# Performance work log

Measured on AMD Instinct MI355X. Metric: run time of the kernel, lower is better.

Reference implementation:

```python
import jax, jax.numpy as jnp
import numpy as np

N0, N1, N2 = 100000, 300000, 200000
C = 64
SLOPE = 0.2

NNZ_A0, NNZ_A1, NNZ_C2, NNZ_B1, NNZ_B2 = 600000, 1200000, 600000, 600000, 600000


def _seg_softmax(logits, seg, n):
    # softmax over nonzero entries of each row (segment = row index)
    m = jax.ops.segment_max(logits, seg, num_segments=n)
    e = jnp.exp(logits - m[seg])
    s = jax.ops.segment_sum(e, seg, num_segments=n)
    return e / s[seg]


def _hbs(x, rows, cols, W, a, n):
    # Higher-order attention block, same rank (m_hop=1, A values = 1)
    m = x @ W                                   # [n, out]
    out = W.shape[1]
    logits = jax.nn.leaky_relu((m @ a[:out])[rows] + (m @ a[out:])[cols], SLOPE)
    att = _seg_softmax(logits, rows, n)         # row-wise softmax on sparsity pattern
    return jax.ops.segment_sum(att[:, None] * m[cols], rows, num_segments=n)


def _hbns(xs, xt, t_rows, s_cols, Ws, Wt, a, n_s, n_t):
    # Higher-order attention block between ranks; neighborhood is [n_t, n_s]
    sm = xs @ Ws                                # [n_s, t_out]
    tm = xt @ Wt                                # [n_t, s_out]
    t_out, s_out = Ws.shape[1], Wt.shape[1]
    # e: source -> target attention logits (row = target); cat([sm_j, tm_i]) @ a
    e = jax.nn.leaky_relu((sm @ a[:t_out])[s_cols] + (tm @ a[t_out:])[t_rows], SLOPE)
    # f: target -> source attention logits (row = source); cat([tm_i, sm_j]) @ a
    f = jax.nn.leaky_relu((tm @ a[:s_out])[t_rows] + (sm @ a[s_out:])[s_cols], SLOPE)
    att_st = _seg_softmax(e, t_rows, n_t)
    att_ts = _seg_softmax(f, s_cols, n_s)
    msg_t = jax.ops.segment_sum(att_st[:, None] * sm[s_cols], t_rows, num_segments=n_t)
    msg_s = jax.ops.segment_sum(att_ts[:, None] * tm[t_rows], s_cols, num_segments=n_s)
    return msg_s, msg_t


def setup_inputs() -> dict:
    key = jax.random.key(0)
    ks = iter(jax.random.split(key, 64))
    sc = 1.0 / np.sqrt(C)
    d = {
        "x_0": jax.random.normal(next(ks), (N0, C), jnp.float32),
        "x_1": jax.random.normal(next(ks), (N1, C), jnp.float32),
        "x_2": jax.random.normal(next(ks), (N2, C), jnp.float32),
        "adj0_rows": jax.random.randint(next(ks), (NNZ_A0,), 0, N0, jnp.int32),
        "adj0_cols": jax.random.randint(next(ks), (NNZ_A0,), 0, N0, jnp.int32),
        "adj1_rows": jax.random.randint(next(ks), (NNZ_A1,), 0, N1, jnp.int32),
        "adj1_cols": jax.random.randint(next(ks), (NNZ_A1,), 0, N1, jnp.int32),
        "coadj2_rows": jax.random.randint(next(ks), (NNZ_C2,), 0, N2, jnp.int32),
        "coadj2_cols": jax.random.randint(next(ks), (NNZ_C2,), 0, N2, jnp.int32),
        "inc1_rows": jax.random.randint(next(ks), (NNZ_B1,), 0, N0, jnp.int32),
        "inc1_cols": jax.random.randint(next(ks), (NNZ_B1,), 0, N1, jnp.int32),
        "inc2_rows": jax.random.randint(next(ks), (NNZ_B2,), 0, N1, jnp.int32),
        "inc2_cols": jax.random.randint(next(ks), (NNZ_B2,), 0, N2, jnp.int32),
    }
    for nm in ["W_hbs0_l1", "W_hbs0_l2", "W_hbs1_l2", "W_hbs2_l2",
               "Ws01_l1", "Wt01_l1", "Ws12_l1", "Wt12_l1",
               "Ws01_l2", "Wt01_l2", "Ws12_l2", "Wt12_l2"]:
        d[nm] = jax.random.normal(next(ks), (C, C), jnp.float32) * sc
    for nm in ["a_hbs0_l1", "a_hbs0_l2", "a_hbs1_l2", "a_hbs2_l2",
               "a01_l1", "a12_l1", "a01_l2", "a12_l2"]:
        d[nm] = jax.random.normal(next(ks), (2 * C,), jnp.float32) * sc
    return d


def reference(x_0, x_1, x_2,
              adj0_rows, adj0_cols, adj1_rows, adj1_cols,
              coadj2_rows, coadj2_cols, inc1_rows, inc1_cols,
              inc2_rows, inc2_cols,
              W_hbs0_l1, a_hbs0_l1, W_hbs0_l2, a_hbs0_l2,
              W_hbs1_l2, a_hbs1_l2, W_hbs2_l2, a_hbs2_l2,
              Ws01_l1, Wt01_l1, a01_l1, Ws12_l1, Wt12_l1, a12_l1,
              Ws01_l2, Wt01_l2, a01_l2, Ws12_l2, Wt12_l2, a12_l2):
    # ---- level 1 ----
    x_0_to_0 = _hbs(x_0, adj0_rows, adj0_cols, W_hbs0_l1, a_hbs0_l1, N0)
    x_0_to_1, x_1_to_0 = _hbns(x_1, x_0, inc1_rows, inc1_cols,
                               Ws01_l1, Wt01_l1, a01_l1, N1, N0)
    x_1_to_2, x_2_to_1 = _hbns(x_2, x_1, inc2_rows, inc2_cols,
                               Ws12_l1, Wt12_l1, a12_l1, N2, N1)
    x_0_l1 = x_0_to_0 + x_1_to_0
    x_1_l1 = x_0_to_1 + x_2_to_1
    x_2_l1 = x_1_to_2
    # ---- level 2 ----
    x_0_to_0 = _hbs(x_0_l1, adj0_rows, adj0_cols, W_hbs0_l2, a_hbs0_l2, N0)
    x_1_to_1 = _hbs(x_1_l1, adj1_rows, adj1_cols, W_hbs1_l2, a_hbs1_l2, N1)
    x_2_to_2 = _hbs(x_2_l1, coadj2_rows, coadj2_cols, W_hbs2_l2, a_hbs2_l2, N2)
    x_0_to_1, _ = _hbns(x_1_l1, x_0_l1, inc1_rows, inc1_cols,
                        Ws01_l2, Wt01_l2, a01_l2, N1, N0)
    x_1_to_2, _ = _hbns(x_2_l1, x_1_l1, inc2_rows, inc2_cols,
                        Ws12_l2, Wt12_l2, a12_l2, N2, N1)
    x_0_out = x_0_to_0
    x_1_out = x_0_to_1 + x_1_to_1
    x_2_out = x_1_to_2 + x_2_to_2
    return x_0_out, x_1_out, x_2_out
```

## Files before the change

kernel.cpp:

```cpp
#include <hip/hip_runtime.h>

#define CN0 100000
#define CN1 300000
#define CN2 200000
#define EA0 600000
#define EA1 1200000
#define EC2 600000
#define EB1 600000
#define EB2 600000
#define TOTSEG (2*CN0 + 3*CN1 + 2*CN2)
#define OVCAP 16384

typedef __attribute__((ext_vector_type(8))) short short8;
typedef __attribute__((ext_vector_type(4))) float f32x4;
typedef __attribute__((ext_vector_type(4))) unsigned short u16x4;

__device__ __forceinline__ float lrelu(float v) { return v >= 0.f ? v : 0.2f * v; }
__device__ __forceinline__ unsigned short btop(float x) {
    return (unsigned short)(__float_as_uint(x) >> 16);
}
__device__ __forceinline__ unsigned short f2bf(float x) {
    unsigned u = __float_as_uint(x);
    return (unsigned short)((u + 0x7FFFu + ((u >> 16) & 1u)) >> 16);
}
__device__ __forceinline__ float bf2f(unsigned short b) {
    return __uint_as_float((unsigned)b << 16);
}

struct Pats {
    const int* seg[7];
    const int* vidx[7];
    int E[7];
    int base[7];
    int K[7];
    int eoff[7];
};

struct MMJob {
    const float* X; const float* W; const float* a;
    unsigned short* Y; float* p; float* q; int nchunk;
};

__device__ __forceinline__ void mm_body(const float* __restrict__ X, const float* __restrict__ W,
                                        const float* __restrict__ a, unsigned short* __restrict__ Yb,
                                        float* __restrict__ p, float* __restrict__ q,
                                        int nchunk, int wid, int nw, int lane) {
    int l15 = lane & 15, lq = lane >> 4;
    short8 bh[4][2], bl[4][2];
#pragma unroll
    for (int t = 0; t < 4; ++t)
#pragma unroll
        for (int h = 0; h < 2; ++h) {
            const float* wp = W + (size_t)(h * 32 + lq * 8) * 64 + 16 * t + l15;
#pragma unroll
            for (int j = 0; j < 8; ++j) {
                float wv = wp[(size_t)j * 64];
                unsigned short hi = btop(wv);
                float rem = wv - __uint_as_float((unsigned)hi << 16);
                bh[t][h][j] = (short)hi;
                bl[t][h][j] = (short)btop(rem);
            }
        }
    float av0[4], av1[4];
#pragma unroll
    for (int t = 0; t < 4; ++t) {
        av0[t] = a[16 * t + l15];
        av1[t] = a[64 + 16 * t + l15];
    }
    for (int c = wid; c < nchunk; c += nw) {
        int base = c * 16;
        f32x4 acc[4];
#pragma unroll
        for (int t = 0; t < 4; ++t) acc[t] = (f32x4){0.f, 0.f, 0.f, 0.f};
#pragma unroll
        for (int h = 0; h < 2; ++h) {
            const f32x4* xp = (const f32x4*)(X + (size_t)(base + l15) * 64 + h * 32 + lq * 8);
            f32x4 x0 = xp[0], x1 = xp[1];
            short8 ah, al;
#pragma unroll
            for (int j = 0; j < 4; ++j) {
                unsigned short h0 = btop(x0[j]);
                float r0 = x0[j] - __uint_as_float((unsigned)h0 << 16);
                ah[j] = (short)h0;
                al[j] = (short)btop(r0);
                unsigned short h1 = btop(x1[j]);
                float r1 = x1[j] - __uint_as_float((unsigned)h1 << 16);
                ah[4 + j] = (short)h1;
                al[4 + j] = (short)btop(r1);
            }
#pragma unroll
            for (int t = 0; t < 4; ++t) {
                acc[t] = __builtin_amdgcn_mfma_f32_16x16x32_bf16(ah, bh[t][h], acc[t], 0, 0, 0);
                acc[t] = __builtin_amdgcn_mfma_f32_16x16x32_bf16(ah, bl[t][h], acc[t], 0, 0, 0);
                acc[t] = __builtin_amdgcn_mfma_f32_16x16x32_bf16(al, bh[t][h], acc[t], 0, 0, 0);
            }
        }
#pragma unroll
        for (int t = 0; t < 4; ++t)
#pragma unroll
            for (int r = 0; r < 4; ++r)
                Yb[(size_t)(base + lq * 4 + r) * 64 + 16 * t + l15] = f2bf(acc[t][r]);
#pragma unroll
        for (int r = 0; r < 4; ++r) {
            float pr = acc[0][r] * av0[0] + acc[1][r] * av0[1] + acc[2][r] * av0[2] + acc[3][r] * av0[3];
            float qr = acc[0][r] * av1[0] + acc[1][r] * av1[1] + acc[2][r] * av1[2] + acc[3][r] * av1[3];
#pragma unroll
            for (int off = 8; off; off >>= 1) {
                pr += __shfl_xor(pr, off, 64);
                qr += __shfl_xor(qr, off, 64);
            }
            if (l15 == 0) {
                p[base + lq * 4 + r] = pr;
                q[base + lq * 4 + r] = qr;
            }
        }
    }
}

__global__ __launch_bounds__(256) void k_l1_fused(
        MMJob j0, MMJob j1, MMJob j2, MMJob j3, MMJob j4,
        Pats P, int* __restrict__ cnt, int* __restrict__ ell,
        int* __restrict__ ovf_gs, int* __restrict__ ovf_vx, int* __restrict__ ovf_n,
        int mmBlocks) {
    int b = blockIdx.x;
    int nm = 5 * mmBlocks;
    int lane = threadIdx.x & 63;
    if (b < nm) {
        int role = b / mmBlocks, rb = b - role * mmBlocks;
        MMJob J = (role == 0) ? j0 : (role == 1) ? j1 : (role == 2) ? j2
                : (role == 3) ? j3 : j4;
        int wid = rb * (blockDim.x >> 6) + (threadIdx.x >> 6);
        int nw = mmBlocks * (blockDim.x >> 6);
        mm_body(J.X, J.W, J.a, J.Y, J.p, J.q, J.nchunk, wid, nw, lane);
    } else {
        int hb = b - nm;
        int pidx = 0, acc = 0;
        for (; pidx < 7; ++pidx) {
            int pb = (P.E[pidx] + 255) >> 8;
            if (hb < acc + pb) break;
            acc += pb;
        }
        if (pidx >= 7) return;
        int e = (hb - acc) * 256 + threadIdx.x;
        if (e >= P.E[pidx]) return;
        int sv = P.seg[pidx][e];
        int gs = P.base[pidx] + sv;
        int vx = P.vidx[pidx][e];
        int r = atomicAdd(&cnt[gs], 1);
        int Kp = P.K[pidx];
        if (r < Kp) {
            ell[(size_t)P.eoff[pidx] + (size_t)sv * Kp + r] = vx;
        } else {
            int o = atomicAdd(ovf_n, 1);
            if (o < OVCAP) { ovf_gs[o] = gs; ovf_vx[o] = vx; }
        }
    }
}

template <int DUAL, int VEC>
__global__ __launch_bounds__(256) void mm64_t(
        const float* __restrict__ X,
        const float* __restrict__ W1, const float* __restrict__ a1,
        unsigned short* __restrict__ Y1, float* __restrict__ p1, float* __restrict__ q1,
        const float* __restrict__ W2, const float* __restrict__ a2,
        unsigned short* __restrict__ Y2, float* __restrict__ p2, float* __restrict__ q2,
        const float* __restrict__ uuv, float* __restrict__ pv, int nchunk) {
    int lane = threadIdx.x & 63;
    int l15 = lane & 15, lq = lane >> 4;
    int wid = blockIdx.x * (blockDim.x >> 6) + (threadIdx.x >> 6);
    int nw = gridDim.x * (blockDim.x >> 6);

    short8 b1h[4][2], b1l[4][2], b2h[4][2], b2l[4][2];
#pragma unroll
    for (int t = 0; t < 4; ++t)
#pragma unroll
        for (int h = 0; h < 2; ++h) {
            const float* wp = W1 + (size_t)(h * 32 + lq * 8) * 64 + 16 * t + l15;
#pragma unroll
            for (int j = 0; j < 8; ++j) {
                float wv = wp[(size_t)j * 64];
                unsigned short hi = btop(wv);
                float rem = wv - __uint_as_float((unsigned)hi << 16);
                b1h[t][h][j] = (short)hi;
                b1l[t][h][j] = (short)btop(rem);
            }
        }
    if (DUAL) {
#pragma unroll
        for (int t = 0; t < 4; ++t)
#pragma unroll
            for (int h = 0; h < 2; ++h) {
                const float* wp = W2 + (size_t)(h * 32 + lq * 8) * 64 + 16 * t + l15;
#pragma unroll
                for (int j = 0; j < 8; ++j) {
                    float wv = wp[(size_t)j * 64];
                    unsigned short hi = btop(wv);
                    float rem = wv - __uint_as_float((unsigned)hi << 16);
                    b2h[t][h][j] = (short)hi;
                    b2l[t][h][j] = (short)btop(rem);
                }
            }
    }
    float a10[4], a11[4], a20[4], a21[4];
#pragma unroll
    for (int t = 0; t < 4; ++t) {
        a10[t] = a1[16 * t + l15];
        a11[t] = a1[64 + 16 * t + l15];
        if (DUAL) { a20[t] = a2[16 * t + l15]; a21[t] = a2[64 + 16 * t + l15]; }
    }
    float uv[16];
    if (VEC) {
#pragma unroll
        for (int h = 0; h < 2; ++h)
#pragma unroll
            for (int j = 0; j < 8; ++j) uv[h * 8 + j] = uuv[h * 32 + lq * 8 + j];
    }

    for (int c = wid; c < nchunk; c += nw) {
        int base = c * 16;
        f32x4 acc1[4], acc2[4];
#pragma unroll
        for (int t = 0; t < 4; ++t) {
            acc1[t] = (f32x4){0.f, 0.f, 0.f, 0.f};
            if (DUAL) acc2[t] = (f32x4){0.f, 0.f, 0.f, 0.f};
        }
        float vp = 0.f;
#pragma unroll
        for (int h = 0; h < 2; ++h) {
            const f32x4* xp = (const f32x4*)(X + (size_t)(base + l15) * 64 + h * 32 + lq * 8);
            f32x4 x0 = xp[0], x1 = xp[1];
            if (VEC) {
#pragma unroll
                for (int j = 0; j < 4; ++j)
                    vp += x0[j] * uv[h * 8 + j] + x1[j] * uv[h * 8 + 4 + j];
            }
            short8 ah, al;
#pragma unroll
            for (int j = 0; j < 4; ++j) {
                unsigned short h0 = btop(x0[j]);
                float r0 = x0[j] - __uint_as_float((unsigned)h0 << 16);
                ah[j] = (short)h0;
                al[j] = (short)btop(r0);
                unsigned short h1 = btop(x1[j]);
                float r1 = x1[j] - __uint_as_float((unsigned)h1 << 16);
                ah[4 + j] = (short)h1;
                al[4 + j] = (short)btop(r1);
            }
#pragma unroll
            for (int t = 0; t < 4; ++t) {
                acc1[t] = __builtin_amdgcn_mfma_f32_16x16x32_bf16(ah, b1h[t][h], acc1[t], 0, 0, 0);
                acc1[t] = __builtin_amdgcn_mfma_f32_16x16x32_bf16(ah, b1l[t][h], acc1[t], 0, 0, 0);
                acc1[t] = __builtin_amdgcn_mfma_f32_16x16x32_bf16(al, b1h[t][h], acc1[t], 0, 0, 0);
                if (DUAL) {
                    acc2[t] = __builtin_amdgcn_mfma_f32_16x16x32_bf16(ah, b2h[t][h], acc2[t], 0, 0, 0);
                    acc2[t] = __builtin_amdgcn_mfma_f32_16x16x32_bf16(ah, b2l[t][h], acc2[t], 0, 0, 0);
                    acc2[t] = __builtin_amdgcn_mfma_f32_16x16x32_bf16(al, b2h[t][h], acc2[t], 0, 0, 0);
                }
            }
        }
#pragma unroll
        for (int t = 0; t < 4; ++t)
#pragma unroll
            for (int r = 0; r < 4; ++r) {
                Y1[(size_t)(base + lq * 4 + r) * 64 + 16 * t + l15] = f2bf(acc1[t][r]);
                if (DUAL) Y2[(size_t)(base + lq * 4 + r) * 64 + 16 * t + l15] = f2bf(acc2[t][r]);
            }
#pragma unroll
        for (int r = 0; r < 4; ++r) {
            float pr = acc1[0][r] * a10[0] + acc1[1][r] * a10[1] + acc1[2][r] * a10[2] + acc1[3][r] * a10[3];
            float qr = acc1[0][r] * a11[0] + acc1[1][r] * a11[1] + acc1[2][r] * a11[2] + acc1[3][r] * a11[3];
#pragma unroll
            for (int off = 8; off; off >>= 1) {
                pr += __shfl_xor(pr, off, 64);
                qr += __shfl_xor(qr, off, 64);
            }
            if (l15 == 0) {
                p1[base + lq * 4 + r] = pr;
                q1[base + lq * 4 + r] = qr;
            }
            if (DUAL) {
                float pr2 = acc2[0][r] * a20[0] + acc2[1][r] * a20[1] + acc2[2][r] * a20[2] + acc2[3][r] * a20[3];
                float qr2 = acc2[0][r] * a21[0] + acc2[1][r] * a21[1] + acc2[2][r] * a21[2] + acc2[3][r] * a21[3];
#pragma unroll
                for (int off = 8; off; off >>= 1) {
                    pr2 += __shfl_xor(pr2, off, 64);
                    qr2 += __shfl_xor(qr2, off, 64);
                }
                if (l15 == 0) {
                    p2[base + lq * 4 + r] = pr2;
                    q2[base + lq * 4 + r] = qr2;
                }
            }
        }
        if (VEC) {
            vp += __shfl_xor(vp, 16, 64);
            vp += __shfl_xor(vp, 32, 64);
            if (lane < 16) pv[base + l15] = vp;
        }
    }
}

__global__ void uvec_k(const float* __restrict__ W, const float* __restrict__ a2c,
                       float* __restrict__ uu) {
    int j = threadIdx.x;
    float s0 = 0.f, s1 = 0.f;
    for (int k = 0; k < 64; ++k) {
        float w = W[j * 64 + k];
        s0 = fmaf(w, a2c[k], s0);
        s1 = fmaf(w, a2c[64 + k], s1);
    }
    uu[j] = s0;
    uu[64 + j] = s1;
}

__device__ __forceinline__ void seg_gather(
    const int* __restrict__ cnt, int base, int K, const int* __restrict__ ellp,
    int s, const float* __restrict__ ps, const float* __restrict__ pv,
    const unsigned short* __restrict__ Mb, int gl, int gbase, f32x4& acc,
    const int* __restrict__ ovf_gs, const int* __restrict__ ovf_vx, int ovn,
    int* exv, int* ec) {
    int gs = base + s;
    int deg = cnt[gs];
    if (deg <= 0) return;
    const int* row = ellp + (size_t)s * K;
    float pss = ps[s];
    if (deg <= K) {
        int v = (gl < deg) ? row[gl] : 0;
        float l = (gl < deg) ? lrelu(pss + pv[v]) : -3.4e38f;
        float mx = l;
#pragma unroll
        for (int off = 8; off; off >>= 1) mx = fmaxf(mx, __shfl_xor(mx, off, 64));
        float ev = (gl < deg) ? __expf(l - mx) : 0.f;
        float ssum = ev;
#pragma unroll
        for (int off = 8; off; off >>= 1) ssum += __shfl_xor(ssum, off, 64);
        float att = ev / ssum;
        for (int t0 = 0; t0 < deg; t0 += 4) {
            float w0 = __shfl(att, gbase + t0, 64), w1 = __shfl(att, gbase + t0 + 1, 64);
            float w2 = __shfl(att, gbase + t0 + 2, 64), w3 = __shfl(att, gbase + t0 + 3, 64);
            int u0 = __shfl(v, gbase + t0, 64), u1 = __shfl(v, gbase + t0 + 1, 64);
            int u2 = __shfl(v, gbase + t0 + 2, 64), u3 = __shfl(v, gbase + t0 + 3, 64);
            u16x4 m0 = *(const u16x4*)(Mb + (size_t)u0 * 64 + gl * 4);
            u16x4 m1 = *(const u16x4*)(Mb + (size_t)u1 * 64 + gl * 4);
            u16x4 m2 = *(const u16x4*)(Mb + (size_t)u2 * 64 + gl * 4);
            u16x4 m3 = *(const u16x4*)(Mb + (size_t)u3 * 64 + gl * 4);
#pragma unroll
            for (int kk = 0; kk < 4; ++kk)
                acc[kk] += w0 * bf2f(m0[kk]) + w1 * bf2f(m1[kk]) +
                           w2 * bf2f(m2[kk]) + w3 * bf2f(m3[kk]);
        }
    } else {
        if (gl == 0) *ec = 0;
        for (int j = gl; j < ovn; j += 16)
            if (ovf_gs[j] == gs) { int k = atomicAdd(ec, 1); if (k < 24) exv[k] = ovf_vx[j]; }
        int m = min(*ec, 24);
        int total = K + m;
        float mx = -3.4e38f;
        for (int j0 = 0; j0 < total; j0 += 16) {
            int idx = j0 + gl;
            int v = (idx < total) ? ((idx < K) ? row[idx] : exv[idx - K]) : 0;
            float l = (idx < total) ? lrelu(pss + pv[v]) : -3.4e38f;
            mx = fmaxf(mx, l);
        }
#pragma unroll
        for (int off = 8; off; off >>= 1) mx = fmaxf(mx, __shfl_xor(mx, off, 64));
        float ssum = 0.f;
        for (int j0 = 0; j0 < total; j0 += 16) {
            int idx = j0 + gl;
            int v = (idx < total) ? ((idx < K) ? row[idx] : exv[idx - K]) : 0;
            ssum += (idx < total) ? __expf(lrelu(pss + pv[v]) - mx) : 0.f;
        }
#pragma unroll
        for (int off = 8; off; off >>= 1) ssum += __shfl_xor(ssum, off, 64);
        float inv = 1.f / ssum;
        for (int j0 = 0; j0 < total; j0 += 16) {
            int idx = j0 + gl;
            int v = (idx < total) ? ((idx < K) ? row[idx] : exv[idx - K]) : 0;
            float ev = (idx < total) ? __expf(lrelu(pss + pv[v]) - mx) * inv : 0.f;
            int cc = min(16, total - j0);
            for (int t = 0; t < cc; ++t) {
                float w = __shfl(ev, gbase + t, 64);
                int vv = __shfl(v, gbase + t, 64);
                const u16x4 mv = *(const u16x4*)(Mb + (size_t)vv * 64 + gl * 4);
#pragma unroll
                for (int kk = 0; kk < 4; ++kk) acc[kk] = fmaf(w, bf2f(mv[kk]), acc[kk]);
            }
        }
    }
}

__global__ void k_attn1(const int* __restrict__ cnt, int base, int K, const int* __restrict__ ellp,
                        const float* __restrict__ ps, const float* __restrict__ pv,
                        const unsigned short* __restrict__ Mb,
                        const int* __restrict__ ovf_gs, const int* __restrict__ ovf_vx,
                        const int* __restrict__ ovf_n,
                        float* __restrict__ out, int nseg) {
    __shared__ int exv[16][24];
    __shared__ int ec[16];
    int lane = threadIdx.x & 63;
    int grp = threadIdx.x >> 4;
    int g = lane >> 4, gl = lane & 15, gbase = g << 4;
    int s = (blockIdx.x * (blockDim.x >> 6) + (threadIdx.x >> 6)) * 4 + g;
    if (s >= nseg) return;
    int ovn = min(*ovf_n, OVCAP);
    f32x4 acc = (f32x4){0.f, 0.f, 0.f, 0.f};
    seg_gather(cnt, base, K, ellp, s, ps, pv, Mb, gl, gbase, acc,
               ovf_gs, ovf_vx, ovn, exv[grp], &ec[grp]);
    *(f32x4*)(out + (size_t)s * 64 + gl * 4) = acc;
}

__global__ void k_attn2(const int* __restrict__ cnt,
                        int baseA, int KA, const int* __restrict__ ellA,
                        const float* __restrict__ psA, const float* __restrict__ pvA,
                        const unsigned short* __restrict__ MbA,
                        int baseB, int KB, const int* __restrict__ ellB,
                        const float* __restrict__ psB, const float* __restrict__ pvB,
                        const unsigned short* __restrict__ MbB,
                        const int* __restrict__ ovf_gs, const int* __restrict__ ovf_vx,
                        const int* __restrict__ ovf_n,
                        float* __restrict__ out, int nseg) {
    __shared__ int exv[16][24];
    __shared__ int ec[16];
    int lane = threadIdx.x & 63;
    int grp = threadIdx.x >> 4;
    int g = lane >> 4, gl = lane & 15, gbase = g << 4;
    int s = (blockIdx.x * (blockDim.x >> 6) + (threadIdx.x >> 6)) * 4 + g;
    if (s >= nseg) return;
    int ovn = min(*ovf_n, OVCAP);
    f32x4 acc = (f32x4){0.f, 0.f, 0.f, 0.f};
    seg_gather(cnt, baseA, KA, ellA, s, psA, pvA, MbA, gl, gbase, acc,
               ovf_gs, ovf_vx, ovn, exv[grp], &ec[grp]);
    seg_gather(cnt, baseB, KB, ellB, s, psB, pvB, MbB, gl, gbase, acc,
               ovf_gs, ovf_vx, ovn, exv[grp], &ec[grp]);
    *(f32x4*)(out + (size_t)s * 64 + gl * 4) = acc;
}

extern "C" void kernel_launch(void* const* d_in, const int* in_sizes, int n_in,
                              void* d_out, int out_size, void* d_ws, size_t ws_size,
                              hipStream_t stream) {
    (void)in_sizes; (void)n_in; (void)ws_size; (void)out_size;
    const float* x0 = (const float*)d_in[0];
    const float* x1 = (const float*)d_in[1];
    const float* x2 = (const float*)d_in[2];
    const int* adj0r = (const int*)d_in[3];
    const int* adj0c = (const int*)d_in[4];
    const int* adj1r = (const int*)d_in[5];
    const int* adj1c = (const int*)d_in[6];
    const int* co2r = (const int*)d_in[7];
    const int* co2c = (const int*)d_in[8];
    const int* i1r = (const int*)d_in[9];
    const int* i1c = (const int*)d_in[10];
    const int* i2r = (const int*)d_in[11];
    const int* i2c = (const int*)d_in[12];
    const float* W_h0_l1 = (const float*)d_in[13];
    const float* W_h0_l2 = (const float*)d_in[14];
    const float* W_h1_l2 = (const float*)d_in[15];
    const float* W_h2_l2 = (const float*)d_in[16];
    const float* Ws01_l1 = (const float*)d_in[17];
    const float* Wt01_l1 = (const float*)d_in[18];
    const float* Ws12_l1 = (const float*)d_in[19];
    const float* Wt12_l1 = (const float*)d_in[20];
    const float* Ws01_l2 = (const float*)d_in[21];
    const float* Wt01_l2 = (const float*)d_in[22];
    const float* Ws12_l2 = (const float*)d_in[23];
    const float* Wt12_l2 = (const float*)d_in[24];
    const float* a_h0_l1 = (const float*)d_in[25];
    const float* a_h0_l2 = (const float*)d_in[26];
    const float* a_h1_l2 = (const float*)d_in[27];
    const float* a_h2_l2 = (const float*)d_in[28];
    const float* a01_l1 = (const float*)d_in[29];
    const float* a12_l1 = (const float*)d_in[30];
    const float* a01_l2 = (const float*)d_in[31];
    const float* a12_l2 = (const float*)d_in[32];

    float* fb = (float*)d_ws;
    float* t0 = fb;              float* t1 = t0 + 300000;
    float* t2 = t1 + 300000;     float* t3 = t2 + 300000;
    float* t4 = t3 + 300000;     float* t5 = t4 + 300000;
    float* t6 = t5 + 300000;     float* t7 = t6 + 300000;
    float* t8 = t7 + 300000;     float* t9 = t8 + 300000;
    float* t10 = t9 + 300000;
    float* uuA = t10 + 300000;
    float* uuB = uuA + 128;
    unsigned short* YA = (unsigned short*)(uuB + 128);
    unsigned short* YB = YA + (size_t)CN0 * 64;
    unsigned short* YC = YB + (size_t)CN1 * 64;
    unsigned short* YD = YC + (size_t)CN0 * 64;
    unsigned short* YE = YD + (size_t)CN2 * 64;
    int* cnt    = (int*)(YE + (size_t)CN1 * 64);
    int* ell    = cnt + TOTSEG;
    int* ovf_gs = ell + 15200000;
    int* ovf_vx = ovf_gs + OVCAP;
    int* ovf_n  = ovf_vx + OVCAP;

    float* r0 = (float*)d_out;
    float* r1 = r0 + (size_t)CN0 * 64;
    float* r2 = r1 + (size_t)CN1 * 64;

    const int bA0 = 0;
    const int bE1 = CN0;
    const int bF1 = 2 * CN0;
    const int bE2 = 2 * CN0 + CN1;
    const int bF2 = 2 * CN0 + 2 * CN1;
    const int bA1 = 2 * CN0 + 2 * CN1 + CN2;
    const int bC2 = 2 * CN0 + 3 * CN1 + CN2;
    Pats P;
    P.seg[0] = adj0r; P.vidx[0] = adj0c; P.E[0] = EA0; P.base[0] = bA0;
    P.seg[1] = i1r;   P.vidx[1] = i1c;   P.E[1] = EB1; P.base[1] = bE1;
    P.seg[2] = i1c;   P.vidx[2] = i1r;   P.E[2] = EB1; P.base[2] = bF1;
    P.seg[3] = i2r;   P.vidx[3] = i2c;   P.E[3] = EB2; P.base[3] = bE2;
    P.seg[4] = i2c;   P.vidx[4] = i2r;   P.E[4] = EB2; P.base[4] = bF2;
    P.seg[5] = adj1r; P.vidx[5] = adj1c; P.E[5] = EA1; P.base[5] = bA1;
    P.seg[6] = co2r;  P.vidx[6] = co2c;  P.E[6] = EC2; P.base[6] = bC2;
    const int Ks[7]   = {14, 14, 8, 8, 10, 12, 10};
    const int Eoff[7] = {0, 1400000, 2800000, 5200000, 7600000, 9600000, 13200000};
    int histBlocks = 0;
    for (int p = 0; p < 7; ++p) {
        P.K[p] = Ks[p];
        P.eoff[p] = Eoff[p];
        histBlocks += (P.E[p] + 255) / 256;
    }

    auto AGG1 = [&](int p, const float* ps, const float* pv, const unsigned short* Mb,
                    float* out, int nseg) {
        k_attn1<<<dim3((nseg + 15) / 16), dim3(256), 0, stream>>>(
            cnt, P.base[p], P.K[p], ell + P.eoff[p], ps, pv, Mb,
            ovf_gs, ovf_vx, ovf_n, out, nseg);
    };
    auto AGG2 = [&](int pA, const float* psA, const float* pvA, const unsigned short* MbA,
                    int pB, const float* psB, const float* pvB, const unsigned short* MbB,
                    float* out, int nseg) {
        k_attn2<<<dim3((nseg + 15) / 16), dim3(256), 0, stream>>>(
            cnt, P.base[pA], P.K[pA], ell + P.eoff[pA], psA, pvA, MbA,
            P.base[pB], P.K[pB], ell + P.eoff[pB], psB, pvB, MbB,
            ovf_gs, ovf_vx, ovf_n, out, nseg);
    };

    hipMemsetAsync(cnt, 0, (size_t)TOTSEG * 4, stream);
    hipMemsetAsync(ovf_n, 0, 4, stream);
    {
        const int mmBlocks = 96;
        MMJob j0 = {x0, W_h0_l1, a_h0_l1, YA, t0, t1, CN0 / 16};
        MMJob j1 = {x1, Ws01_l1, a01_l1, YB, t2, t3, CN1 / 16};
        MMJob j2 = {x0, Wt01_l1, a01_l1, YC, t4, t5, CN0 / 16};
        MMJob j3 = {x2, Ws12_l1, a12_l1, YD, t6, t7, CN2 / 16};
        MMJob j4 = {x1, Wt12_l1, a12_l1, YE, t8, t9, CN1 / 16};
        k_l1_fused<<<dim3(5 * mmBlocks + histBlocks), dim3(256), 0, stream>>>(
            j0, j1, j2, j3, j4, P, cnt, ell, ovf_gs, ovf_vx, ovf_n, mmBlocks);
    }

    AGG2(0, t0, t1, YA, 1, t5, t2, YB, r0, CN0);
    AGG2(2, t3, t4, YC, 3, t9, t6, YD, r1, CN1);
    AGG1(4, t7, t8, YE, r2, CN2);

    uvec_k<<<dim3(1), dim3(64), 0, stream>>>(Ws01_l2, a01_l2, uuA);
    uvec_k<<<dim3(1), dim3(64), 0, stream>>>(Ws12_l2, a12_l2, uuB);
    {
        int blocks0 = min(1024, (CN0 / 16 + 3) / 4);
        int blocks1 = min(1024, (CN1 / 16 + 3) / 4);
        int blocks2 = min(1024, (CN2 / 16 + 3) / 4);
        mm64_t<1, 0><<<dim3(blocks0), dim3(256), 0, stream>>>(
            r0, W_h0_l2, a_h0_l2, YA, t0, t1,
            Wt01_l2, a01_l2, YC, t4, t5, nullptr, nullptr, CN0 / 16);
        mm64_t<1, 1><<<dim3(blocks1), dim3(256), 0, stream>>>(
            r1, W_h1_l2, a_h1_l2, YB, t2, t3,
            Wt12_l2, a12_l2, YE, t8, t5, uuA + 64, t6, CN1 / 16);
        mm64_t<0, 1><<<dim3(blocks2), dim3(256), 0, stream>>>(
            r2, W_h2_l2, a_h2_l2, YD, t7, t9,
            nullptr, nullptr, nullptr, nullptr, nullptr, uuB + 64, t10, CN2 / 16);
    }
    AGG1(0, t0, t1, YA, r0, CN0);
    AGG2(5, t2, t3, YB, 2, t6, t4, YC, r1, CN1);
    AGG2(6, t7, t9, YD, 4, t10, t8, YE, r2, CN2);
}
```

Baseline: 851.3 us.

## Merge aggregation and level-2 matmul launches into multi-task fused kernels

Replaces the three level-1 aggregation launches with one multi-task kernel, which also computes the two u-vectors in an extra block so the separate uvec launches go away. The three level-2 matmul launches become one kernel that dispatches on block index, and the three level-2 aggregation launches become one more multi-task kernel. This cuts launch count and the tail gaps between small kernels. It also changes the ELL row capacities (K values, wider for some patterns, narrower for others) and enlarges the ELL buffer to match. Narrower rows can push more edges into the bounded overflow list, and the changed layout affects padding and memory traffic.

```diff
diff --git a/kernel.cpp b/kernel.cpp
--- a/kernel.cpp
+++ b/kernel.cpp
@@ -39,6 +39,21 @@
 struct MMJob {
     const float* X; const float* W; const float* a;
     unsigned short* Y; float* p; float* q; int nchunk;
+};
+
+struct MMT {
+    const float* X;
+    const float* W1; const float* a1; unsigned short* Y1; float* p1; float* q1;
+    const float* W2; const float* a2; unsigned short* Y2; float* p2; float* q2;
+    const float* uuv; float* pv; int nchunk;
+};
+
+struct AggTask {
+    int baseA, KA, eoffA;
+    const float* psA; const float* pvA; const unsigned short* MbA;
+    int baseB, KB, eoffB;
+    const float* psB; const float* pvB; const unsigned short* MbB;
+    float* out; int nseg;
 };
 
 __device__ __forceinline__ void mm_body(const float* __restrict__ X, const float* __restrict__ W,
@@ -158,24 +173,18 @@
 }
 
 template <int DUAL, int VEC>
-__global__ __launch_bounds__(256) void mm64_t(
-        const float* __restrict__ X,
-        const float* __restrict__ W1, const float* __restrict__ a1,
-        unsigned short* __restrict__ Y1, float* __restrict__ p1, float* __restrict__ q1,
-        const float* __restrict__ W2, const float* __restrict__ a2,
-        unsigned short* __restrict__ Y2, float* __restrict__ p2, float* __restrict__ q2,
-        const float* __restrict__ uuv, float* __restrict__ pv, int nchunk) {
+__device__ __forceinline__ void mm_l2_body(const MMT& T, int lb, int nb) {
     int lane = threadIdx.x & 63;
     int l15 = lane & 15, lq = lane >> 4;
-    int wid = blockIdx.x * (blockDim.x >> 6) + (threadIdx.x >> 6);
-    int nw = gridDim.x * (blockDim.x >> 6);
+    int wid = lb * (blockDim.x >> 6) + (threadIdx.x >> 6);
+    int nw = nb * (blockDim.x >> 6);
 
     short8 b1h[4][2], b1l[4][2], b2h[4][2], b2l[4][2];
 #pragma unroll
     for (int t = 0; t < 4; ++t)
 #pragma unroll
         for (int h = 0; h < 2; ++h) {
-            const float* wp = W1 + (size_t)(h * 32 + lq * 8) * 64 + 16 * t + l15;
+            const float* wp = T.W1 + (size_t)(h * 32 + lq * 8) * 64 + 16 * t + l15;
 #pragma unroll
             for (int j = 0; j < 8; ++j) {
                 float wv = wp[(size_t)j * 64];
@@ -190,7 +199,7 @@
         for (int t = 0; t < 4; ++t)
 #pragma unroll
             for (int h = 0; h < 2; ++h) {
-                const float* wp = W2 + (size_t)(h * 32 + lq * 8) * 64 + 16 * t + l15;
+                const float* wp = T.W2 + (size_t)(h * 32 + lq * 8) * 64 + 16 * t + l15;
 #pragma unroll
                 for (int j = 0; j < 8; ++j) {
                     float wv = wp[(size_t)j * 64];
@@ -204,19 +213,19 @@
     float a10[4], a11[4], a20[4], a21[4];
 #pragma unroll
     for (int t = 0; t < 4; ++t) {
-        a10[t] = a1[16 * t + l15];
-        a11[t] = a1[64 + 16 * t + l15];
-        if (DUAL) { a20[t] = a2[16 * t + l15]; a21[t] = a2[64 + 16 * t + l15]; }
+        a10[t] = T.a1[16 * t + l15];
+        a11[t] = T.a1[64 + 16 * t + l15];
+        if (DUAL) { a20[t] = T.a2[16 * t + l15]; a21[t] = T.a2[64 + 16 * t + l15]; }
     }
     float uv[16];
     if (VEC) {
 #pragma unroll
         for (int h = 0; h < 2; ++h)
 #pragma unroll
-            for (int j = 0; j < 8; ++j) uv[h * 8 + j] = uuv[h * 32 + lq * 8 + j];
-    }
-
-    for (int c = wid; c < nchunk; c += nw) {
+            for (int j = 0; j < 8; ++j) uv[h * 8 + j] = T.uuv[h * 32 + lq * 8 + j];
+    }
+
+    for (int c = wid; c < T.nchunk; c += nw) {
         int base = c * 16;
         f32x4 acc1[4], acc2[4];
 #pragma unroll
@@ -227,7 +236,7 @@
         float vp = 0.f;
 #pragma unroll
         for (int h = 0; h < 2; ++h) {
-            const f32x4* xp = (const f32x4*)(X + (size_t)(base + l15) * 64 + h * 32 + lq * 8);
+            const f32x4* xp = (const f32x4*)(T.X + (size_t)(base + l15) * 64 + h * 32 + lq * 8);
             f32x4 x0 = xp[0], x1 = xp[1];
             if (VEC) {
 #pragma unroll
@@ -262,8 +271,8 @@
         for (int t = 0; t < 4; ++t)
 #pragma unroll
             for (int r = 0; r < 4; ++r) {
-                Y1[(size_t)(base + lq * 4 + r) * 64 + 16 * t + l15] = f2bf(acc1[t][r]);
-                if (DUAL) Y2[(size_t)(base + lq * 4 + r) * 64 + 16 * t + l15] = f2bf(acc2[t][r]);
+                T.Y1[(size_t)(base + lq * 4 + r) * 64 + 16 * t + l15] = f2bf(acc1[t][r]);
+                if (DUAL) T.Y2[(size_t)(base + lq * 4 + r) * 64 + 16 * t + l15] = f2bf(acc2[t][r]);
             }
 #pragma unroll
         for (int r = 0; r < 4; ++r) {
@@ -275,8 +284,8 @@
                 qr += __shfl_xor(qr, off, 64);
             }
             if (l15 == 0) {
-                p1[base + lq * 4 + r] = pr;
-                q1[base + lq * 4 + r] = qr;
+                T.p1[base + lq * 4 + r] = pr;
+                T.q1[base + lq * 4 + r] = qr;
             }
             if (DUAL) {
                 float pr2 = acc2[0][r] * a20[0] + acc2[1][r] * a20[1] + acc2[2][r] * a20[2] + acc2[3][r] * a20[3];
@@ -287,30 +296,24 @@
                     qr2 += __shfl_xor(qr2, off, 64);
                 }
                 if (l15 == 0) {
-                    p2[base + lq * 4 + r] = pr2;
-                    q2[base + lq * 4 + r] = qr2;
+                    T.p2[base + lq * 4 + r] = pr2;
+                    T.q2[base + lq * 4 + r] = qr2;
                 }
             }
         }
         if (VEC) {
             vp += __shfl_xor(vp, 16, 64);
             vp += __shfl_xor(vp, 32, 64);
-            if (lane < 16) pv[base + l15] = vp;
-        }
-    }
-}
-
-__global__ void uvec_k(const float* __restrict__ W, const float* __restrict__ a2c,
-                       float* __restrict__ uu) {
-    int j = threadIdx.x;
-    float s0 = 0.f, s1 = 0.f;
-    for (int k = 0; k < 64; ++k) {
-        float w = W[j * 64 + k];
-        s0 = fmaf(w, a2c[k], s0);
-        s1 = fmaf(w, a2c[64 + k], s1);
-    }
-    uu[j] = s0;
-    uu[64 + j] = s1;
+            if (lane < 16) T.pv[base + l15] = vp;
+        }
+    }
+}
+
+__global__ __launch_bounds__(256) void k_mm3(MMT A, MMT B, MMT C, int nb0, int nb1, int nb2) {
+    int b = blockIdx.x;
+    if (b < nb0) mm_l2_body<1, 0>(A, b, nb0);
+    else if (b < nb0 + nb1) mm_l2_body<1, 1>(B, b - nb0, nb1);
+    else mm_l2_body<0, 1>(C, b - nb0 - nb1, nb2);
 }
 
 __device__ __forceinline__ void seg_gather(
@@ -389,50 +392,53 @@
     }
 }
 
-__global__ void k_attn1(const int* __restrict__ cnt, int base, int K, const int* __restrict__ ellp,
-                        const float* __restrict__ ps, const float* __restrict__ pv,
-                        const unsigned short* __restrict__ Mb,
-                        const int* __restrict__ ovf_gs, const int* __restrict__ ovf_vx,
-                        const int* __restrict__ ovf_n,
-                        float* __restrict__ out, int nseg) {
+__global__ __launch_bounds__(256) void k_agg3(
+        AggTask T0, AggTask T1, AggTask T2, int nb0, int nb1, int nb2,
+        const int* __restrict__ cnt, const int* __restrict__ ell,
+        const int* __restrict__ ovf_gs, const int* __restrict__ ovf_vx,
+        const int* __restrict__ ovf_n,
+        int doUU, const float* __restrict__ WsA, const float* __restrict__ aA,
+        float* __restrict__ uuA,
+        const float* __restrict__ WsB, const float* __restrict__ aB,
+        float* __restrict__ uuB) {
     __shared__ int exv[16][24];
     __shared__ int ec[16];
+    int b = blockIdx.x;
+    int nAgg = nb0 + nb1 + nb2;
+    if (b >= nAgg) {
+        if (!doUU || threadIdx.x >= 128) return;
+        int j = threadIdx.x & 63;
+        const float* W = (threadIdx.x < 64) ? WsA : WsB;
+        const float* a2c = (threadIdx.x < 64) ? aA : aB;
+        float* uu = (threadIdx.x < 64) ? uuA : uuB;
+        float s0 = 0.f, s1 = 0.f;
+        for (int k = 0; k < 64; ++k) {
+            float w = W[j * 64 + k];
+            s0 = fmaf(w, a2c[k], s0);
+            s1 = fmaf(w, a2c[64 + k], s1);
+        }
+        uu[j] = s0;
+        uu[64 + j] = s1;
+        return;
+    }
+    const AggTask* T;
+    int lb;
+    if (b < nb0) { T = &T0; lb = b; }
+    else if (b < nb0 + nb1) { T = &T1; lb = b - nb0; }
+    else { T = &T2; lb = b - nb0 - nb1; }
     int lane = threadIdx.x & 63;
     int grp = threadIdx.x >> 4;
     int g = lane >> 4, gl = lane & 15, gbase = g << 4;
-    int s = (blockIdx.x * (blockDim.x >> 6) + (threadIdx.x >> 6)) * 4 + g;
-    if (s >= nseg) return;
+    int s = (lb * (blockDim.x >> 6) + (threadIdx.x >> 6)) * 4 + g;
+    if (s >= T->nseg) return;
     int ovn = min(*ovf_n, OVCAP);
     f32x4 acc = (f32x4){0.f, 0.f, 0.f, 0.f};
-    seg_gather(cnt, base, K, ellp, s, ps, pv, Mb, gl, gbase, acc,
-               ovf_gs, ovf_vx, ovn, exv[grp], &ec[grp]);
-    *(f32x4*)(out + (size_t)s * 64 + gl * 4) = acc;
-}
-
-__global__ void k_attn2(const int* __restrict__ cnt,
-                        int baseA, int KA, const int* __restrict__ ellA,
-                        const float* __restrict__ psA, const float* __restrict__ pvA,
-                        const unsigned short* __restrict__ MbA,
-                        int baseB, int KB, const int* __restrict__ ellB,
-                        const float* __restrict__ psB, const float* __restrict__ pvB,
-                        const unsigned short* __restrict__ MbB,
-                        const int* __restrict__ ovf_gs, const int* __restrict__ ovf_vx,
-                        const int* __restrict__ ovf_n,
-                        float* __restrict__ out, int nseg) {
-    __shared__ int exv[16][24];
-    __shared__ int ec[16];
-    int lane = threadIdx.x & 63;
-    int grp = threadIdx.x >> 4;
-    int g = lane >> 4, gl = lane & 15, gbase = g << 4;
-    int s = (blockIdx.x * (blockDim.x >> 6) + (threadIdx.x >> 6)) * 4 + g;
-    if (s >= nseg) return;
-    int ovn = min(*ovf_n, OVCAP);
-    f32x4 acc = (f32x4){0.f, 0.f, 0.f, 0.f};
-    seg_gather(cnt, baseA, KA, ellA, s, psA, pvA, MbA, gl, gbase, acc,
-               ovf_gs, ovf_vx, ovn, exv[grp], &ec[grp]);
-    seg_gather(cnt, baseB, KB, ellB, s, psB, pvB, MbB, gl, gbase, acc,
-               ovf_gs, ovf_vx, ovn, exv[grp], &ec[grp]);
-    *(f32x4*)(out + (size_t)s * 64 + gl * 4) = acc;
+    seg_gather(cnt, T->baseA, T->KA, ell + T->eoffA, s, T->psA, T->pvA, T->MbA,
+               gl, gbase, acc, ovf_gs, ovf_vx, ovn, exv[grp], &ec[grp]);
+    if (T->baseB >= 0)
+        seg_gather(cnt, T->baseB, T->KB, ell + T->eoffB, s, T->psB, T->pvB, T->MbB,
+                   gl, gbase, acc, ovf_gs, ovf_vx, ovn, exv[grp], &ec[grp]);
+    *(f32x4*)(T->out + (size_t)s * 64 + gl * 4) = acc;
 }
 
 extern "C" void kernel_launch(void* const* d_in, const int* in_sizes, int n_in,
@@ -489,7 +495,7 @@
     unsigned short* YE = YD + (size_t)CN2 * 64;
     int* cnt    = (int*)(YE + (size_t)CN1 * 64);
     int* ell    = cnt + TOTSEG;
-    int* ovf_gs = ell + 15200000;
+    int* ovf_gs = ell + 16000000;
     int* ovf_vx = ovf_gs + OVCAP;
     int* ovf_n  = ovf_vx + OVCAP;
 
@@ -512,29 +518,14 @@
     P.seg[4] = i2c;   P.vidx[4] = i2r;   P.E[4] = EB2; P.base[4] = bF2;
     P.seg[5] = adj1r; P.vidx[5] = adj1c; P.E[5] = EA1; P.base[5] = bA1;
     P.seg[6] = co2r;  P.vidx[6] = co2c;  P.E[6] = EC2; P.base[6] = bC2;
-    const int Ks[7]   = {14, 14, 8, 8, 10, 12, 10};
-    const int Eoff[7] = {0, 1400000, 2800000, 5200000, 7600000, 9600000, 13200000};
+    const int Ks[7]   = {16, 16, 8, 8, 8, 16, 8};
+    const int Eoff[7] = {0, 1600000, 3200000, 5600000, 8000000, 9600000, 14400000};
     int histBlocks = 0;
     for (int p = 0; p < 7; ++p) {
         P.K[p] = Ks[p];
         P.eoff[p] = Eoff[p];
         histBlocks += (P.E[p] + 255) / 256;
     }
-
-    auto AGG1 = [&](int p, const float* ps, const float* pv, const unsigned short* Mb,
-                    float* out, int nseg) {
-        k_attn1<<<dim3((nseg + 15) / 16), dim3(256), 0, stream>>>(
-            cnt, P.base[p], P.K[p], ell + P.eoff[p], ps, pv, Mb,
-            ovf_gs, ovf_vx, ovf_n, out, nseg);
-    };
-    auto AGG2 = [&](int pA, const float* psA, const float* pvA, const unsigned short* MbA,
-                    int pB, const float* psB, const float* pvB, const unsigned short* MbB,
-                    float* out, int nseg) {
-        k_attn2<<<dim3((nseg + 15) / 16), dim3(256), 0, stream>>>(
-            cnt, P.base[pA], P.K[pA], ell + P.eoff[pA], psA, pvA, MbA,
-            P.base[pB], P.K[pB], ell + P.eoff[pB], psB, pvB, MbB,
-            ovf_gs, ovf_vx, ovf_n, out, nseg);
-    };
 
     hipMemsetAsync(cnt, 0, (size_t)TOTSEG * 4, stream);
     hipMemsetAsync(ovf_n, 0, 4, stream);
@@ -549,27 +540,39 @@
             j0, j1, j2, j3, j4, P, cnt, ell, ovf_gs, ovf_vx, ovf_n, mmBlocks);
     }
 
-    AGG2(0, t0, t1, YA, 1, t5, t2, YB, r0, CN0);
-    AGG2(2, t3, t4, YC, 3, t9, t6, YD, r1, CN1);
-    AGG1(4, t7, t8, YE, r2, CN2);
-
-    uvec_k<<<dim3(1), dim3(64), 0, stream>>>(Ws01_l2, a01_l2, uuA);
-    uvec_k<<<dim3(1), dim3(64), 0, stream>>>(Ws12_l2, a12_l2, uuB);
     {
-        int blocks0 = min(1024, (CN0 / 16 + 3) / 4);
-        int blocks1 = min(1024, (CN1 / 16 + 3) / 4);
-        int blocks2 = min(1024, (CN2 / 16 + 3) / 4);
-        mm64_t<1, 0><<<dim3(blocks0), dim3(256), 0, stream>>>(
-            r0, W_h0_l2, a_h0_l2, YA, t0, t1,
-            Wt01_l2, a01_l2, YC, t4, t5, nullptr, nullptr, CN0 / 16);
-        mm64_t<1, 1><<<dim3(blocks1), dim3(256), 0, stream>>>(
-            r1, W_h1_l2, a_h1_l2, YB, t2, t3,
-            Wt12_l2, a12_l2, YE, t8, t5, uuA + 64, t6, CN1 / 16);
-        mm64_t<0, 1><<<dim3(blocks2), dim3(256), 0, stream>>>(
-            r2, W_h2_l2, a_h2_l2, YD, t7, t9,
-            nullptr, nullptr, nullptr, nullptr, nullptr, uuB + 64, t10, CN2 / 16);
-    }
-    AGG1(0, t0, t1, YA, r0, CN0);
-    AGG2(5, t2, t3, YB, 2, t6, t4, YC, r1, CN1);
-    AGG2(6, t7, t9, YD, 4, t10, t8, YE, r2, CN2);
-}
+        AggTask T0 = {bA0, 16, Eoff[0], t0, t1, YA,
+                      bE1, 16, Eoff[1], t5, t2, YB, r0, CN0};
+        AggTask T1 = {bF1, 8, Eoff[2], t3, t4, YC,
+                      bE2, 8, Eoff[3], t9, t6, YD, r1, CN1};
+        AggTask T2 = {bF2, 8, Eoff[4], t7, t8, YE,
+                      -1, 0, 0, nullptr, nullptr, nullptr, r2, CN2};
+        int nb0 = (CN0 + 15) / 16, nb1 = (CN1 + 15) / 16, nb2 = (CN2 + 15) / 16;
+        k_agg3<<<dim3(nb0 + nb1 + nb2 + 1), dim3(256), 0, stream>>>(
+            T0, T1, T2, nb0, nb1, nb2, cnt, ell, ovf_gs, ovf_vx, ovf_n,
+            1, Ws01_l2, a01_l2, uuA, Ws12_l2, a12_l2, uuB);
+    }
+
+    {
+        MMT A = {r0, W_h0_l2, a_h0_l2, YA, t0, t1,
+                 Wt01_l2, a01_l2, YC, t4, t5, nullptr, nullptr, CN0 / 16};
+        MMT B = {r1, W_h1_l2, a_h1_l2, YB, t2, t3,
+                 Wt12_l2, a12_l2, YE, t8, t5, uuA + 64, t6, CN1 / 16};
+        MMT C = {r2, W_h2_l2, a_h2_l2, YD, t7, t9,
+                 nullptr, nullptr, nullptr, nullptr, nullptr, uuB + 64, t10, CN2 / 16};
+        k_mm3<<<dim3(384 + 1024 + 640), dim3(256), 0, stream>>>(A, B, C, 384, 1024, 640);
+    }
+
+    {
+        AggTask T0 = {bA0, 16, Eoff[0], t0, t1, YA,
+                      -1, 0, 0, nullptr, nullptr, nullptr, r0, CN0};
+        AggTask T1 = {bA1, 16, Eoff[5], t2, t3, YB,
+                      bF1, 8, Eoff[2], t6, t4, YC, r1, CN1};
+        AggTask T2 = {bC2, 8, Eoff[6], t7, t9, YD,
+                      bF2, 8, Eoff[4], t10, t8, YE, r2, CN2};
+        int nb0 = (CN0 + 15) / 16, nb1 = (CN1 + 15) / 16, nb2 = (CN2 + 15) / 16;
+        k_agg3<<<dim3(nb0 + nb1 + nb2), dim3(256), 0, stream>>>(
+            T0, T1, T2, nb0, nb1, nb2, cnt, ell, ovf_gs, ovf_vx, ovf_n,
+            0, nullptr, nullptr, nullptr, nullptr, nullptr, nullptr);
+    }
+}
```

Result: faster. 832.4 us (-2.2%).
